# Kernel optimization log

Hardware: AMD Instinct MI355X
Metric: run time of the kernel (lower is better)

The kernel has to match this reference:

```python
import jax, jax.numpy as jnp
import numpy as np

N_NODES = 100000
N_EDGES = 1600000
N_GRAPHS = 64
F_IN = 128
HEADS = 4
C = 16
HID = HEADS * C  # 64
N_HIDDEN_LAYERS = 6
NUM_CLASSES = 10
NEG_SLOPE = 0.2


def _gat_layer(h_in, src, dst, W, a_src, a_dst, b):
    # h_in: [N, F]; W: [F, H*C]; a_src/a_dst: [H, C]; b: [H*C]
    N = h_in.shape[0]
    h = (h_in @ W).reshape(N, HEADS, C)                      # [N,H,C]
    alpha_s = jnp.sum(h * a_src, axis=-1)                    # [N,H]
    alpha_d = jnp.sum(h * a_dst, axis=-1)                    # [N,H]
    e = jax.nn.leaky_relu(alpha_s[src] + alpha_d[dst], NEG_SLOPE)  # [E,H]
    # per-destination softmax (self-loops guarantee every node has an in-edge)
    m = jax.ops.segment_max(e, dst, num_segments=N)
    e = jnp.exp(e - m[dst])
    denom = jax.ops.segment_sum(e, dst, num_segments=N)
    w = e / (denom[dst] + 1e-16)                             # [E,H]
    msg = h[src] * w[:, :, None]                             # [E,H,C]
    out = jax.ops.segment_sum(msg, dst, num_segments=N)      # [N,H,C]
    return out.reshape(N, HID) + b


def setup_inputs() -> dict:
    key = jax.random.key(0)
    ks = jax.random.split(key, 16)
    x = jax.random.normal(ks[0], (N_NODES, F_IN), dtype=jnp.float32)
    edge_index = jax.random.randint(ks[1], (2, N_EDGES), 0, N_NODES, dtype=jnp.int64)
    batch = jnp.sort(jax.random.randint(ks[2], (N_NODES,), 0, N_GRAPHS, dtype=jnp.int64))

    def glorot(k, shape):
        fan = shape[0] + shape[-1]
        return jax.random.uniform(k, shape, jnp.float32, -1.0, 1.0) * np.sqrt(6.0 / fan)

    W_in = glorot(ks[3], (F_IN, HID))
    asrc_in = glorot(ks[4], (HEADS, C))
    adst_in = glorot(ks[5], (HEADS, C))
    b_in = jnp.zeros((HID,), jnp.float32)

    W_h = glorot(ks[6], (N_HIDDEN_LAYERS, HID, HID))
    asrc_h = glorot(ks[7], (N_HIDDEN_LAYERS, HEADS, C))
    adst_h = glorot(ks[8], (N_HIDDEN_LAYERS, HEADS, C))
    b_h = jnp.zeros((N_HIDDEN_LAYERS, HID), jnp.float32)

    W1 = glorot(ks[9], (HID, 2 * C))
    b1 = jnp.zeros((2 * C,), jnp.float32)
    W2 = glorot(ks[10], (2 * C, NUM_CLASSES))
    b2 = jnp.zeros((NUM_CLASSES,), jnp.float32)

    return {"x": x, "edge_index": edge_index, "batch": batch,
            "W_in": W_in, "asrc_in": asrc_in, "adst_in": adst_in, "b_in": b_in,
            "W_h": W_h, "asrc_h": asrc_h, "adst_h": adst_h, "b_h": b_h,
            "W1": W1, "b1": b1, "W2": W2, "b2": b2}


def reference(x, edge_index, batch, W_in, asrc_in, adst_in, b_in,
              W_h, asrc_h, adst_h, b_h, W1, b1, W2, b2):
    N = x.shape[0]
    loops = jnp.arange(N, dtype=edge_index.dtype)
    src = jnp.concatenate([edge_index[0], loops])  # add self-loops (PyG default)
    dst = jnp.concatenate([edge_index[1], loops])

    h = jax.nn.relu(_gat_layer(x, src, dst, W_in, asrc_in, adst_in, b_in))
    for i in range(N_HIDDEN_LAYERS):
        h = jax.nn.relu(_gat_layer(h, src, dst, W_h[i], asrc_h[i], adst_h[i], b_h[i]))

    g = jax.ops.segment_max(h, batch, num_segments=N_GRAPHS)  # global_max_pool [G, HID]
    g = jax.nn.relu(g @ W1 + b1)
    return g @ W2 + b2
```

## Files before the change

kernel.cpp:

```cpp
#include <hip/hip_runtime.h>
#include <hip/hip_bf16.h>

#define NN 100000
#define NE 1600000
#define ET 1700000
#define NG 64
#define F_IN 128
#define HID 64
#define NLAYERS 6
#define NEG 0.2f
#define NPART 8
#define PBLK 256
#define PNN (NN / NPART)
#define DCAP 64

typedef __attribute__((ext_vector_type(8))) short bf16x8;
typedef __attribute__((ext_vector_type(4))) float f32x4;

static __device__ __forceinline__ unsigned short f2bf(float f) {
    __hip_bfloat16 b = __float2bfloat16(f);
    return *reinterpret_cast<unsigned short*>(&b);
}
static __device__ __forceinline__ float bf2f(unsigned short u) {
    __hip_bfloat16 b = *reinterpret_cast<__hip_bfloat16*>(&u);
    return __bfloat162float(b);
}

__global__ __launch_bounds__(256) void k_scatter(const int* __restrict__ ei,
                                                 int* __restrict__ counts,
                                                 int* __restrict__ csr) {
    const int part = blockIdx.x & (NPART - 1);
    const int sub  = blockIdx.x >> 3;
    const int lo = part * PNN, hi = lo + PNN;
    const int S = PBLK * 256;
    for (int e0 = sub * 256 + threadIdx.x; e0 < ET; e0 += 4 * S) {
        int e[4], d[4];
        #pragma unroll
        for (int u = 0; u < 4; ++u) {
            e[u] = e0 + u * S;
            d[u] = (e[u] < ET) ? ((e[u] < NE) ? ei[NE + e[u]] : (e[u] - NE)) : -1;
        }
        #pragma unroll
        for (int u = 0; u < 4; ++u) {
            if (d[u] >= lo && d[u] < hi) {
                int src = (e[u] < NE) ? ei[e[u]] : d[u];
                int pos = atomicAdd(&counts[d[u]], 1);
                if (pos < DCAP) csr[(d[u] << 6) + pos] = src;
            }
        }
    }
}

__global__ __launch_bounds__(256) void k_gemm_mfma128(
    const float* __restrict__ X,
    const float* __restrict__ W,
    unsigned short* __restrict__ hw)
{
    __shared__ unsigned short xs[64][136];
    __shared__ unsigned short Wt[64][136];
    const int t = threadIdx.x;
    const int w = t >> 6, lane = t & 63;
    const int n0 = blockIdx.x * 64;

    #pragma unroll
    for (int u = 0; u < 8; ++u) {
        int i = t + u * 256;
        int c4 = (i >> 7) * 4, r = i & 127;
        float4 v = *reinterpret_cast<const float4*>(&W[(size_t)r * 64 + c4]);
        Wt[c4 + 0][r] = f2bf(v.x);
        Wt[c4 + 1][r] = f2bf(v.y);
        Wt[c4 + 2][r] = f2bf(v.z);
        Wt[c4 + 3][r] = f2bf(v.w);
    }
    #pragma unroll
    for (int u = 0; u < 8; ++u) {
        int i = t + u * 256;
        int row = i >> 5, q = i & 31;
        int gn = n0 + row;
        float4 v = (gn < NN)
            ? *reinterpret_cast<const float4*>(&X[(size_t)gn * 128 + q * 4])
            : make_float4(0.f, 0.f, 0.f, 0.f);
        xs[row][q * 4 + 0] = f2bf(v.x);
        xs[row][q * 4 + 1] = f2bf(v.y);
        xs[row][q * 4 + 2] = f2bf(v.z);
        xs[row][q * 4 + 3] = f2bf(v.w);
    }
    __syncthreads();

    const int arow = w * 16 + (lane & 15);
    const int ak = (lane >> 4) * 8;
    f32x4 acc[4] = {};
    #pragma unroll
    for (int kk = 0; kk < 4; ++kk) {
        bf16x8 afrag = *reinterpret_cast<const bf16x8*>(&xs[arow][kk * 32 + ak]);
        #pragma unroll
        for (int ct = 0; ct < 4; ++ct) {
            bf16x8 bfrag = *reinterpret_cast<const bf16x8*>(&Wt[ct * 16 + (lane & 15)][kk * 32 + ak]);
            acc[ct] = __builtin_amdgcn_mfma_f32_16x16x32_bf16(afrag, bfrag, acc[ct], 0, 0, 0);
        }
    }

    const int c = lane & 15;
    const int r0 = w * 16 + ((lane >> 4) << 2);
    #pragma unroll
    for (int ct = 0; ct < 4; ++ct) {
        #pragma unroll
        for (int reg = 0; reg < 4; ++reg) {
            int node = n0 + r0 + reg;
            if (node < NN) hw[(size_t)node * 64 + ct * 16 + c] = f2bf(acc[ct][reg]);
        }
    }
}

__global__ __launch_bounds__(256) void k_gemm_mfma(
    const unsigned short* __restrict__ A,
    const float* __restrict__ W,
    unsigned short* __restrict__ hw)
{
    __shared__ unsigned short Wt[64][72];
    const int t = threadIdx.x;
    const int w = t >> 6, lane = t & 63;
    const int n0 = blockIdx.x * 64;

    #pragma unroll
    for (int u = 0; u < 4; ++u) {
        int i = t + u * 256;
        int r = i >> 4, c4 = (i & 15) * 4;
        float4 v = *reinterpret_cast<const float4*>(&W[(size_t)r * 64 + c4]);
        Wt[c4 + 0][r] = f2bf(v.x);
        Wt[c4 + 1][r] = f2bf(v.y);
        Wt[c4 + 2][r] = f2bf(v.z);
        Wt[c4 + 3][r] = f2bf(v.w);
    }
    __syncthreads();

    const int arow = n0 + w * 16 + (lane & 15);
    const int arc = (arow < NN) ? arow : 0;
    const int ak = (lane >> 4) * 8;
    bf16x8 afrag[2];
    #pragma unroll
    for (int kk = 0; kk < 2; ++kk)
        afrag[kk] = *reinterpret_cast<const bf16x8*>(&A[(size_t)arc * 64 + kk * 32 + ak]);

    f32x4 acc[4] = {};
    #pragma unroll
    for (int ct = 0; ct < 4; ++ct) {
        #pragma unroll
        for (int kk = 0; kk < 2; ++kk) {
            bf16x8 bfrag = *reinterpret_cast<const bf16x8*>(&Wt[ct * 16 + (lane & 15)][kk * 32 + ak]);
            acc[ct] = __builtin_amdgcn_mfma_f32_16x16x32_bf16(afrag[kk], bfrag, acc[ct], 0, 0, 0);
        }
    }

    const int c = lane & 15;
    const int r0 = w * 16 + ((lane >> 4) << 2);
    #pragma unroll
    for (int ct = 0; ct < 4; ++ct) {
        #pragma unroll
        for (int reg = 0; reg < 4; ++reg) {
            int node = n0 + r0 + reg;
            if (node < NN) hw[(size_t)node * 64 + ct * 16 + c] = f2bf(acc[ct][reg]);
        }
    }
}

__global__ __launch_bounds__(256) void k_alpha(
    const unsigned short* __restrict__ hw,
    const float* __restrict__ asrc,
    const float* __restrict__ adst,
    float* __restrict__ as_,
    float* __restrict__ ad_)
{
    int t = blockIdx.x * 256 + threadIdx.x;
    if (t >= NN * 4) return;
    int h = t & 3;
    const bf16x8* row = reinterpret_cast<const bf16x8*>(&hw[((unsigned)(t >> 2) << 6) + (unsigned)(h << 4)]);
    bf16x8 v0 = row[0], v1 = row[1];
    float vs = 0.f, vd = 0.f;
    #pragma unroll
    for (int j = 0; j < 8; ++j) {
        float f = bf2f((unsigned short)v0[j]);
        vs += f * asrc[h * 16 + j];
        vd += f * adst[h * 16 + j];
    }
    #pragma unroll
    for (int j = 0; j < 8; ++j) {
        float f = bf2f((unsigned short)v1[j]);
        vs += f * asrc[h * 16 + 8 + j];
        vd += f * adst[h * 16 + 8 + j];
    }
    as_[t] = vs;
    ad_[t] = vd;
}

__global__ __launch_bounds__(256) void k_aggregate(
    const unsigned short* __restrict__ hw,
    const float* __restrict__ as_,
    const float* __restrict__ ad_,
    const int* __restrict__ counts,
    const int* __restrict__ csr,
    const float* __restrict__ bias,
    unsigned short* __restrict__ outA)
{
    __shared__ float pls[4][DCAP][4];
    __shared__ int   sls[4][DCAP];
    const int wv = threadIdx.x >> 6;
    int wave = (blockIdx.x * blockDim.x + threadIdx.x) >> 6;
    int lane = threadIdx.x & 63;
    if (wave >= NN) return;
    const int n = wave;
    const int beg = n << 6;
    int deg = counts[n];
    deg = (deg < DCAP) ? deg : DCAP;
    const int h1 = lane & 3;
    const int sl = lane >> 2;
    const float adn1 = ad_[(unsigned)n * 4u + (unsigned)h1];

    float m = -1e30f;
    for (int j = sl; j < deg; j += 16) {
        int s = csr[beg + j];
        float e = as_[(unsigned)s * 4u + (unsigned)h1] + adn1;
        e = (e > 0.f) ? e : NEG * e;
        if (h1 == 0) sls[wv][j] = s;
        pls[wv][j][h1] = e;
        m = fmaxf(m, e);
    }
    #pragma unroll
    for (int off = 4; off < 64; off <<= 1)
        m = fmaxf(m, __shfl_xor(m, off));

    float l = 0.f;
    for (int j = sl; j < deg; j += 16) {
        float p = __expf(pls[wv][j][h1] - m);
        pls[wv][j][h1] = p;
        l += p;
    }
    #pragma unroll
    for (int off = 4; off < 64; off <<= 1)
        l += __shfl_xor(l, off);
    const float inv_l = 1.f / (l + 1e-16f);

    const int c16 = lane & 15;
    const int eg  = lane >> 4;
    const int hh  = c16 >> 2;
    const float il2 = __shfl(inv_l, hh);
    float a0 = 0.f, a1 = 0.f, a2 = 0.f, a3 = 0.f;
    for (int i = 0; i < deg; i += 4) {
        int e = i + eg;
        bool act = e < deg;
        int ec = act ? e : 0;
        int s = sls[wv][ec];
        float p = act ? pls[wv][ec][hh] : 0.f;
        ushort4 uv = *reinterpret_cast<const ushort4*>(&hw[((unsigned)s << 6) + (unsigned)(c16 << 2)]);
        a0 += p * bf2f(uv.x);
        a1 += p * bf2f(uv.y);
        a2 += p * bf2f(uv.z);
        a3 += p * bf2f(uv.w);
    }
    a0 += __shfl_xor(a0, 16); a0 += __shfl_xor(a0, 32);
    a1 += __shfl_xor(a1, 16); a1 += __shfl_xor(a1, 32);
    a2 += __shfl_xor(a2, 16); a2 += __shfl_xor(a2, 32);
    a3 += __shfl_xor(a3, 16); a3 += __shfl_xor(a3, 32);
    if (eg == 0) {
        float4 bv = *reinterpret_cast<const float4*>(&bias[c16 * 4]);
        float o0 = a0 * il2 + bv.x;
        float o1 = a1 * il2 + bv.y;
        float o2 = a2 * il2 + bv.z;
        float o3 = a3 * il2 + bv.w;
        ushort4 ov;
        ov.x = f2bf((o0 > 0.f) ? o0 : 0.f);
        ov.y = f2bf((o1 > 0.f) ? o1 : 0.f);
        ov.z = f2bf((o2 > 0.f) ? o2 : 0.f);
        ov.w = f2bf((o3 > 0.f) ? o3 : 0.f);
        *reinterpret_cast<ushort4*>(&outA[((unsigned)n << 6) + (unsigned)(c16 << 2)]) = ov;
    }
}

__global__ void k_pool(const unsigned short* __restrict__ h, const int* __restrict__ batch,
                       unsigned int* __restrict__ g) {
    int wave = (blockIdx.x * blockDim.x + threadIdx.x) >> 6;
    int lane = threadIdx.x & 63;
    int n0 = wave * 32;
    if (n0 >= NN) return;
    int n1 = n0 + 32; if (n1 > NN) n1 = NN;
    int cg = batch[n0];
    float m = 0.f;
    for (int n = n0; n < n1; ++n) {
        int gi = batch[n];
        if (gi != cg) {
            atomicMax(&g[cg * 64 + lane], __float_as_uint(m));
            m = 0.f; cg = gi;
        }
        m = fmaxf(m, bf2f(h[((unsigned)n << 6) | (unsigned)lane]));
    }
    atomicMax(&g[cg * 64 + lane], __float_as_uint(m));
}

__global__ void k_head(const unsigned int* __restrict__ gbits,
                       const float* __restrict__ W1, const float* __restrict__ b1,
                       const float* __restrict__ W2, const float* __restrict__ b2,
                       float* __restrict__ out) {
    __shared__ float gs[NG * 64];
    __shared__ float z1[NG * 32];
    int t = threadIdx.x;
    for (int i = t; i < NG * 64; i += 256) gs[i] = __uint_as_float(gbits[i]);
    __syncthreads();
    for (int i = t; i < NG * 32; i += 256) {
        int gi = i >> 5, c = i & 31;
        float acc = b1[c];
        for (int k = 0; k < 64; ++k) acc += gs[gi * 64 + k] * W1[k * 32 + c];
        z1[i] = (acc > 0.f) ? acc : 0.f;
    }
    __syncthreads();
    for (int i = t; i < NG * 10; i += 256) {
        int gi = i / 10, c = i % 10;
        float acc = b2[c];
        for (int k = 0; k < 32; ++k) acc += z1[gi * 32 + k] * W2[k * 10 + c];
        out[i] = acc;
    }
}

extern "C" void kernel_launch(void* const* d_in, const int* in_sizes, int n_in,
                              void* d_out, int out_size, void* d_ws, size_t ws_size,
                              hipStream_t stream) {
    const float* x       = (const float*)d_in[0];
    const int*   ei      = (const int*)d_in[1];
    const int*   batch   = (const int*)d_in[2];
    const float* W_in    = (const float*)d_in[3];
    const float* asrc_in = (const float*)d_in[4];
    const float* adst_in = (const float*)d_in[5];
    const float* b_in    = (const float*)d_in[6];
    const float* W_hid   = (const float*)d_in[7];
    const float* asrc_h  = (const float*)d_in[8];
    const float* adst_h  = (const float*)d_in[9];
    const float* b_hid   = (const float*)d_in[10];
    const float* W1      = (const float*)d_in[11];
    const float* b1      = (const float*)d_in[12];
    const float* W2      = (const float*)d_in[13];
    const float* b2      = (const float*)d_in[14];
    float* out = (float*)d_out;

    char* base = (char*)d_ws;
    size_t off = 0;
    auto alloc = [&](size_t bytes) -> char* {
        char* p = base + off;
        off += (bytes + 255) & ~size_t(255);
        return p;
    };
    unsigned short* A  = (unsigned short*)alloc((size_t)NN * 64 * 2);
    unsigned short* Bf = (unsigned short*)alloc((size_t)NN * 64 * 2);
    float* as_    = (float*)alloc((size_t)NN * 4 * 4);
    float* ad_    = (float*)alloc((size_t)NN * 4 * 4);
    int*   counts = (int*)alloc((size_t)NN * 4);
    int*   csr    = (int*)alloc((size_t)NN * DCAP * 4);
    unsigned int* g = (unsigned int*)alloc((size_t)NG * 64 * 4);

    hipMemsetAsync(counts, 0, (size_t)NN * 4, stream);
    hipMemsetAsync(g, 0, (size_t)NG * 64 * 4, stream);

    k_scatter<<<NPART * PBLK, 256, 0, stream>>>(ei, counts, csr);

    const int gemm_blocks = (NN + 63) / 64;
    const int node_blocks = (NN * 64 + 255) / 256;
    const int alpha_blocks = (NN * 4 + 255) / 256;

    k_gemm_mfma128<<<gemm_blocks, 256, 0, stream>>>(x, W_in, Bf);
    k_alpha<<<alpha_blocks, 256, 0, stream>>>(Bf, asrc_in, adst_in, as_, ad_);
    k_aggregate<<<node_blocks, 256, 0, stream>>>(Bf, as_, ad_, counts, csr, b_in, A);

    for (int i = 0; i < NLAYERS; ++i) {
        k_gemm_mfma<<<gemm_blocks, 256, 0, stream>>>(A, W_hid + (size_t)i * 64 * 64, Bf);
        k_alpha<<<alpha_blocks, 256, 0, stream>>>(Bf, asrc_h + (size_t)i * 64, adst_h + (size_t)i * 64, as_, ad_);
        k_aggregate<<<node_blocks, 256, 0, stream>>>(Bf, as_, ad_, counts, csr, b_hid + (size_t)i * 64, A);
    }

    int pool_waves = (NN + 31) / 32;
    int pool_blocks = (pool_waves * 64 + 255) / 256;
    k_pool<<<pool_blocks, 256, 0, stream>>>(A, batch, g);
    k_head<<<1, 256, 0, stream>>>(g, W1, b1, W2, b2, out);
}
```

Baseline: 682.7 us.

## Fold attention logits into GEMM via precomputed W·a projection columns

Precomputes W·a_src and W·a_dst per layer in a small kernel, then has each GEMM compute the per-head attention logits as an extra MFMA tile alongside the feature projection. This removes the separate k_alpha kernel launches and their re-read of the bf16 hidden features every layer. In exchange the logits now come from bf16-rounded inputs and weights rather than from the rounded projected features, which changes rounding slightly, and each GEMM does one extra MFMA tile per k-step.

```diff
diff --git a/kernel.cpp b/kernel.cpp
--- a/kernel.cpp
+++ b/kernel.cpp
@@ -51,13 +51,38 @@
     }
 }
 
+__global__ void k_waux(const float* __restrict__ W_in,
+                       const float* __restrict__ asrc_in, const float* __restrict__ adst_in,
+                       const float* __restrict__ W_hid,
+                       const float* __restrict__ asrc_h, const float* __restrict__ adst_h,
+                       float* __restrict__ waux) {
+    int t = blockIdx.x * 256 + threadIdx.x;
+    if (t >= 1024 + NLAYERS * 512) return;
+    int layer, k, j;
+    if (t < 1024) { layer = -1; k = t >> 3; j = t & 7; }
+    else { int r = t - 1024; layer = r >> 9; int q = r & 511; k = q >> 3; j = q & 7; }
+    int h = j & 3;
+    const float* W = (layer < 0) ? W_in : W_hid + (size_t)layer * 64 * 64;
+    const float* a = (layer < 0) ? ((j >= 4) ? adst_in : asrc_in)
+                                 : ((j >= 4) ? adst_h + (size_t)layer * 64
+                                             : asrc_h + (size_t)layer * 64);
+    float s = 0.f;
+    #pragma unroll
+    for (int c = 0; c < 16; ++c) s += W[(size_t)k * 64 + h * 16 + c] * a[h * 16 + c];
+    waux[t] = s;
+}
+
 __global__ __launch_bounds__(256) void k_gemm_mfma128(
     const float* __restrict__ X,
     const float* __restrict__ W,
-    unsigned short* __restrict__ hw)
+    const float* __restrict__ waux,
+    unsigned short* __restrict__ hw,
+    float* __restrict__ as_,
+    float* __restrict__ ad_)
 {
     __shared__ unsigned short xs[64][136];
     __shared__ unsigned short Wt[64][136];
+    __shared__ unsigned short Wa[16][136];
     const int t = threadIdx.x;
     const int w = t >> 6, lane = t & 63;
     const int n0 = blockIdx.x * 64;
@@ -71,6 +96,18 @@
         Wt[c4 + 1][r] = f2bf(v.y);
         Wt[c4 + 2][r] = f2bf(v.z);
         Wt[c4 + 3][r] = f2bf(v.w);
+    }
+    #pragma unroll
+    for (int u = 0; u < 4; ++u) {
+        int i = t + u * 256;
+        int k = i >> 3, j = i & 7;
+        Wa[j][k] = f2bf(waux[(size_t)k * 8 + j]);
+    }
+    #pragma unroll
+    for (int u = 4; u < 8; ++u) {
+        int i = t + u * 256 - 1024;
+        int j = 8 + (i >> 7), k = i & 127;
+        Wa[j][k] = 0;
     }
     #pragma unroll
     for (int u = 0; u < 8; ++u) {
@@ -90,6 +127,7 @@
     const int arow = w * 16 + (lane & 15);
     const int ak = (lane >> 4) * 8;
     f32x4 acc[4] = {};
+    f32x4 acc5 = {};
     #pragma unroll
     for (int kk = 0; kk < 4; ++kk) {
         bf16x8 afrag = *reinterpret_cast<const bf16x8*>(&xs[arow][kk * 32 + ak]);
@@ -98,6 +136,8 @@
             bf16x8 bfrag = *reinterpret_cast<const bf16x8*>(&Wt[ct * 16 + (lane & 15)][kk * 32 + ak]);
             acc[ct] = __builtin_amdgcn_mfma_f32_16x16x32_bf16(afrag, bfrag, acc[ct], 0, 0, 0);
         }
+        bf16x8 bfa = *reinterpret_cast<const bf16x8*>(&Wa[lane & 15][kk * 32 + ak]);
+        acc5 = __builtin_amdgcn_mfma_f32_16x16x32_bf16(afrag, bfa, acc5, 0, 0, 0);
     }
 
     const int c = lane & 15;
@@ -110,14 +150,28 @@
             if (node < NN) hw[(size_t)node * 64 + ct * 16 + c] = f2bf(acc[ct][reg]);
         }
     }
+    if (c < 8) {
+        #pragma unroll
+        for (int reg = 0; reg < 4; ++reg) {
+            int node = n0 + r0 + reg;
+            if (node < NN) {
+                if (c < 4) as_[node * 4 + c] = acc5[reg];
+                else       ad_[node * 4 + (c - 4)] = acc5[reg];
+            }
+        }
+    }
 }
 
 __global__ __launch_bounds__(256) void k_gemm_mfma(
     const unsigned short* __restrict__ A,
     const float* __restrict__ W,
-    unsigned short* __restrict__ hw)
+    const float* __restrict__ waux,
+    unsigned short* __restrict__ hw,
+    float* __restrict__ as_,
+    float* __restrict__ ad_)
 {
     __shared__ unsigned short Wt[64][72];
+    __shared__ unsigned short Wa[16][72];
     const int t = threadIdx.x;
     const int w = t >> 6, lane = t & 63;
     const int n0 = blockIdx.x * 64;
@@ -132,6 +186,18 @@
         Wt[c4 + 2][r] = f2bf(v.z);
         Wt[c4 + 3][r] = f2bf(v.w);
     }
+    #pragma unroll
+    for (int u = 0; u < 2; ++u) {
+        int i = t + u * 256;
+        int k = i >> 3, j = i & 7;
+        Wa[j][k] = f2bf(waux[(size_t)k * 8 + j]);
+    }
+    #pragma unroll
+    for (int u = 0; u < 2; ++u) {
+        int i = t + u * 256;
+        int j = 8 + (i >> 6), k = i & 63;
+        Wa[j][k] = 0;
+    }
     __syncthreads();
 
     const int arow = n0 + w * 16 + (lane & 15);
@@ -143,13 +209,16 @@
         afrag[kk] = *reinterpret_cast<const bf16x8*>(&A[(size_t)arc * 64 + kk * 32 + ak]);
 
     f32x4 acc[4] = {};
-    #pragma unroll
-    for (int ct = 0; ct < 4; ++ct) {
-        #pragma unroll
-        for (int kk = 0; kk < 2; ++kk) {
+    f32x4 acc5 = {};
+    #pragma unroll
+    for (int kk = 0; kk < 2; ++kk) {
+        #pragma unroll
+        for (int ct = 0; ct < 4; ++ct) {
             bf16x8 bfrag = *reinterpret_cast<const bf16x8*>(&Wt[ct * 16 + (lane & 15)][kk * 32 + ak]);
             acc[ct] = __builtin_amdgcn_mfma_f32_16x16x32_bf16(afrag[kk], bfrag, acc[ct], 0, 0, 0);
         }
+        bf16x8 bfa = *reinterpret_cast<const bf16x8*>(&Wa[lane & 15][kk * 32 + ak]);
+        acc5 = __builtin_amdgcn_mfma_f32_16x16x32_bf16(afrag[kk], bfa, acc5, 0, 0, 0);
     }
 
     const int c = lane & 15;
@@ -162,35 +231,16 @@
             if (node < NN) hw[(size_t)node * 64 + ct * 16 + c] = f2bf(acc[ct][reg]);
         }
     }
-}
-
-__global__ __launch_bounds__(256) void k_alpha(
-    const unsigned short* __restrict__ hw,
-    const float* __restrict__ asrc,
-    const float* __restrict__ adst,
-    float* __restrict__ as_,
-    float* __restrict__ ad_)
-{
-    int t = blockIdx.x * 256 + threadIdx.x;
-    if (t >= NN * 4) return;
-    int h = t & 3;
-    const bf16x8* row = reinterpret_cast<const bf16x8*>(&hw[((unsigned)(t >> 2) << 6) + (unsigned)(h << 4)]);
-    bf16x8 v0 = row[0], v1 = row[1];
-    float vs = 0.f, vd = 0.f;
-    #pragma unroll
-    for (int j = 0; j < 8; ++j) {
-        float f = bf2f((unsigned short)v0[j]);
-        vs += f * asrc[h * 16 + j];
-        vd += f * adst[h * 16 + j];
-    }
-    #pragma unroll
-    for (int j = 0; j < 8; ++j) {
-        float f = bf2f((unsigned short)v1[j]);
-        vs += f * asrc[h * 16 + 8 + j];
-        vd += f * adst[h * 16 + 8 + j];
-    }
-    as_[t] = vs;
-    ad_[t] = vd;
+    if (c < 8) {
+        #pragma unroll
+        for (int reg = 0; reg < 4; ++reg) {
+            int node = n0 + r0 + reg;
+            if (node < NN) {
+                if (c < 4) as_[node * 4 + c] = acc5[reg];
+                else       ad_[node * 4 + (c - 4)] = acc5[reg];
+            }
+        }
+    }
 }
 
 __global__ __launch_bounds__(256) void k_aggregate(
@@ -353,24 +403,25 @@
     float* ad_    = (float*)alloc((size_t)NN * 4 * 4);
     int*   counts = (int*)alloc((size_t)NN * 4);
     int*   csr    = (int*)alloc((size_t)NN * DCAP * 4);
+    float* waux   = (float*)alloc((size_t)(1024 + NLAYERS * 512) * 4);
     unsigned int* g = (unsigned int*)alloc((size_t)NG * 64 * 4);
 
     hipMemsetAsync(counts, 0, (size_t)NN * 4, stream);
     hipMemsetAsync(g, 0, (size_t)NG * 64 * 4, stream);
 
     k_scatter<<<NPART * PBLK, 256, 0, stream>>>(ei, counts, csr);
+    k_waux<<<(1024 + NLAYERS * 512 + 255) / 256, 256, 0, stream>>>(
+        W_in, asrc_in, adst_in, W_hid, asrc_h, adst_h, waux);
 
     const int gemm_blocks = (NN + 63) / 64;
     const int node_blocks = (NN * 64 + 255) / 256;
-    const int alpha_blocks = (NN * 4 + 255) / 256;
-
-    k_gemm_mfma128<<<gemm_blocks, 256, 0, stream>>>(x, W_in, Bf);
-    k_alpha<<<alpha_blocks, 256, 0, stream>>>(Bf, asrc_in, adst_in, as_, ad_);
+
+    k_gemm_mfma128<<<gemm_blocks, 256, 0, stream>>>(x, W_in, waux, Bf, as_, ad_);
     k_aggregate<<<node_blocks, 256, 0, stream>>>(Bf, as_, ad_, counts, csr, b_in, A);
 
     for (int i = 0; i < NLAYERS; ++i) {
-        k_gemm_mfma<<<gemm_blocks, 256, 0, stream>>>(A, W_hid + (size_t)i * 64 * 64, Bf);
-        k_alpha<<<alpha_blocks, 256, 0, stream>>>(Bf, asrc_h + (size_t)i * 64, adst_h + (size_t)i * 64, as_, ad_);
+        k_gemm_mfma<<<gemm_blocks, 256, 0, stream>>>(
+            A, W_hid + (size_t)i * 64 * 64, waux + 1024 + (size_t)i * 512, Bf, as_, ad_);
         k_aggregate<<<node_blocks, 256, 0, stream>>>(Bf, as_, ad_, counts, csr, b_hid + (size_t)i * 64, A);
     }
 
```

Result: faster. 650.7 us (-4.7%).
